# Kernel optimization log

Hardware: AMD Instinct MI355X
Metric: run time of the kernel (lower is better)

The kernel has to match this reference:

```python
import jax, jax.numpy as jnp
import numpy as np

B, T, TM = 4, 1024, 1500
D_MODEL, D_FFN, H, D_HEAD, D_MEM = 1024, 4096, 16, 64, 1024
EPS = 1e-5


def layernorm(x, g):
    m = jnp.mean(x, axis=-1, keepdims=True)
    xc = x - m
    v = jnp.mean(xc * xc, axis=-1, keepdims=True)
    return xc * jax.lax.rsqrt(v + EPS) * g


def setup_inputs() -> dict:
    key = jax.random.key(0)
    ks = jax.random.split(key, 12)
    s = lambda fan_in: 1.0 / np.sqrt(fan_in)
    return {
        "x": jax.random.normal(ks[0], (B, T, D_MODEL), jnp.float32),
        "encoder_output": jax.random.normal(ks[1], (B, TM, D_MEM), jnp.float32),
        "encoder_mask": jax.random.randint(ks[2], (B, TM), 0, 2).astype(bool),
        "w_qkv": jax.random.normal(ks[3], (D_MODEL, 3 * H * D_HEAD), jnp.float32) * s(D_MODEL),
        "w_o_sa": jax.random.normal(ks[4], (H * D_HEAD, D_MODEL), jnp.float32) * s(H * D_HEAD),
        "w_q": jax.random.normal(ks[5], (D_MODEL, H * D_HEAD), jnp.float32) * s(D_MODEL),
        "w_kv": jax.random.normal(ks[6], (D_MEM, 2 * H * D_HEAD), jnp.float32) * s(D_MEM),
        "w_o_xa": jax.random.normal(ks[7], (H * D_HEAD, D_MODEL), jnp.float32) * s(H * D_HEAD),
        "w_ff1": jax.random.normal(ks[8], (D_MODEL, D_FFN), jnp.float32) * s(D_MODEL),
        "w_ff2": jax.random.normal(ks[9], (D_FFN, D_MODEL), jnp.float32) * s(D_FFN),
        "g_sa": jnp.ones((D_MODEL,), jnp.float32),
        "g_xaq": jnp.ones((D_MODEL,), jnp.float32),
        "g_xam": jnp.ones((D_MEM,), jnp.float32),
        "g_ff": jnp.ones((D_MODEL,), jnp.float32),
    }


def reference(x, encoder_output, encoder_mask, w_qkv, w_o_sa, w_q, w_kv, w_o_xa,
              w_ff1, w_ff2, g_sa, g_xaq, g_xam, g_ff):
    b, t, _ = x.shape
    scale = D_HEAD ** -0.5

    # ---- causal self-attention ----
    residual = x
    xn = layernorm(x, g_sa)
    qkv = (xn @ w_qkv).reshape(b, t, 3, H, D_HEAD)
    q, k, v = qkv[:, :, 0], qkv[:, :, 1], qkv[:, :, 2]  # (B,T,H,D)
    scores = jnp.einsum('bqhd,bkhd->bhqk', q, k) * scale
    causal = jnp.tril(jnp.ones((t, t), x.dtype))
    scores = scores + (1.0 - causal) * -1e9
    attn = jax.nn.softmax(scores, axis=-1)
    sa = jnp.einsum('bhqk,bkhd->bqhd', attn, v).reshape(b, t, H * D_HEAD)
    x = residual + sa @ w_o_sa

    # ---- cross-attention ----
    residual = x
    qn = layernorm(x, g_xaq)
    mn = layernorm(encoder_output, g_xam)
    tq, tm = t, mn.shape[1]
    qx = (qn @ w_q).reshape(b, tq, H, D_HEAD)
    kvx = (mn @ w_kv).reshape(b, tm, 2, H, D_HEAD)
    kx, vx = kvx[:, :, 0], kvx[:, :, 1]
    xs = jnp.einsum('bqhd,bkhd->bhqk', qx, kx) * scale
    xs = jnp.where(encoder_mask[:, None, None, :], xs, -jnp.inf)
    xattn = jax.nn.softmax(xs, axis=-1)
    xa = jnp.einsum('bhqk,bkhd->bqhd', xattn, vx).reshape(b, tq, H * D_HEAD)
    x = residual + xa @ w_o_xa

    # ---- pointwise FFN (kernel_size=1 conv == linear) ----
    residual = x
    h = layernorm(x, g_ff)
    h = jax.nn.gelu(h @ w_ff1, approximate=True) @ w_ff2
    x = residual + h
    return (x, k, v)
```

## Files before the change

### kernel.cpp

```cpp
#include <hip/hip_runtime.h>
#include <hip/hip_bf16.h>
#include <cstdint>
#include <cstddef>


typedef __attribute__((ext_vector_type(4))) float f32x4;
typedef __attribute__((ext_vector_type(8))) short s8v;
typedef __attribute__((ext_vector_type(2))) unsigned uint2v;

#define DEVI __device__ __forceinline__

DEVI short f2bf(float f) {
  union { float f; unsigned u; } x; x.f = f;
  unsigned r = x.u + 0x7fffu + ((x.u >> 16) & 1u);
  return (short)(r >> 16);
}
DEVI unsigned cvtpk_bf2(float lo, float hi) {
  unsigned r;
  asm("v_cvt_pk_bf16_f32 %0, %1, %2" : "=v"(r) : "v"(lo), "v"(hi));
  return r;
}
DEVI float fexp2(float x) {
  float r;
  asm("v_exp_f32 %0, %1" : "=v"(r) : "v"(x));
  return r;
}
DEVI float fmax3(float a, float b, float c) {
  float r;
  asm("v_max3_f32 %0, %1, %2, %3" : "=v"(r) : "v"(a), "v"(b), "v"(c));
  return r;
}
DEVI float bpermf(int srclane, float v) {
  union { float f; int i; } x; x.f = v;
  x.i = __builtin_amdgcn_ds_bpermute(srclane << 2, x.i);
  return x.f;
}
DEVI void gload_lds16(const void* g, void* l) {
  __builtin_amdgcn_global_load_lds((const __attribute__((address_space(1))) void*)g,
                                   (__attribute__((address_space(3))) void*)l,
                                   16, 0, 0);
}

DEVI void xcd_swizzle(int& bx, int& by) {
  int gx = gridDim.x, gy = gridDim.y;
  int nxy = gx * gy, chunk = nxy >> 3;
  int orig = blockIdx.y * gx + blockIdx.x;
  int gid = (orig & 7) * chunk + (orig >> 3);
  int full = gy << 3, nfull = gx >> 3, lim = nfull * full;
  if (gid < lim) {
    int band = gid / full, r = gid - band * full;
    bx = (band << 3) + (r & 7);
    by = r >> 3;
  } else {
    int r = gid - lim, w = gx - (nfull << 3);
    bx = (nfull << 3) + r % w;
    by = r / w;
  }
}

__global__ __launch_bounds__(256) void k_prep(
    const float* __restrict__ wqkv, const float* __restrict__ wosa,
    const float* __restrict__ wq,   const float* __restrict__ wkv,
    const float* __restrict__ woxa, const float* __restrict__ wff1,
    const float* __restrict__ wff2,
    short* __restrict__ wqkv_t, short* __restrict__ wosa_t,
    short* __restrict__ wq_t,   short* __restrict__ wkv_t,
    short* __restrict__ woxa_t, short* __restrict__ wff1_t,
    short* __restrict__ wff2_t,
    const int* __restrict__ mask, unsigned long long* __restrict__ mbits) {
  int id = blockIdx.x;
  const float* w; short* wt; int K, N, tx, r;
  if (id < 3072)       { w = wqkv; wt = wqkv_t; K = 1024; N = 3072; tx = 96;  r = id; }
  else if (id < 4096)  { w = wosa; wt = wosa_t; K = 1024; N = 1024; tx = 32;  r = id - 3072; }
  else if (id < 5120)  { w = wq;   wt = wq_t;   K = 1024; N = 1024; tx = 32;  r = id - 4096; }
  else if (id < 7168)  { w = wkv;  wt = wkv_t;  K = 1024; N = 2048; tx = 64;  r = id - 5120; }
  else if (id < 8192)  { w = woxa; wt = woxa_t; K = 1024; N = 1024; tx = 32;  r = id - 7168; }
  else if (id < 12288) { w = wff1; wt = wff1_t; K = 1024; N = 4096; tx = 128; r = id - 8192; }
  else if (id < 16384) { w = wff2; wt = wff2_t; K = 4096; N = 1024; tx = 32;  r = id - 12288; }
  else {
    int t = threadIdx.x;
    if (t < 96) {
      int b = t / 24, wd = t % 24;
      unsigned long long v = 0;
      const int* mb = mask + (size_t)b * 1500;
      for (int j = 0; j < 64; j++) {
        int k = wd * 64 + j;
        if (k < 1500 && mb[k]) v |= (1ull << j);
      }
      mbits[b * 24 + wd] = v;
    }
    return;
  }
  __shared__ float tile[32][33];
  int n0 = (r % tx) * 32, k0 = (r / tx) * 32;
  int t = threadIdx.x;
  int row = t >> 3, c4 = (t & 7) * 4;
  *(f32x4*)&tile[row][c4] = *(const f32x4*)(w + (size_t)(k0 + row) * N + n0 + c4);
  __syncthreads();
  float v0 = tile[c4 + 0][row], v1 = tile[c4 + 1][row];
  float v2 = tile[c4 + 2][row], v3 = tile[c4 + 3][row];
  uint2v o = {cvtpk_bf2(v0, v1), cvtpk_bf2(v2, v3)};
  *(uint2v*)(wt + (size_t)(n0 + row) * K + k0 + c4) = o;
}

__global__ __launch_bounds__(256) void k_vtrans(
    const short* __restrict__ src, int srs, int coff,
    short* __restrict__ dst, int T, int Tp) {
  __shared__ short tile[32][72];
  int bh = blockIdx.y, b = bh >> 4, h = bh & 15;
  int t0 = blockIdx.x * 32;
  const short* sB = src + (size_t)b * T * srs + coff + h * 64;
  short* dB = dst + (size_t)bh * 64 * Tp;
  int t = threadIdx.x;
  int r = t >> 3, c = (t & 7) * 8;
  int tr = t0 + r; if (tr > T - 1) tr = T - 1;
  *(s8v*)&tile[r][c] = *(const s8v*)(sB + (size_t)tr * srs + c);
  __syncthreads();
  int d = t & 63, ch = t >> 6;
  s8v o;
#pragma unroll
  for (int j = 0; j < 8; j++) o[j] = tile[ch * 8 + j][d];
  *(s8v*)(dB + (size_t)d * Tp + t0 + ch * 8) = o;
}

__global__ __launch_bounds__(256) void k_ln2(
    const float* __restrict__ x, const float* __restrict__ gx,
    short* __restrict__ ox,
    const float* __restrict__ e, const float* __restrict__ ge,
    short* __restrict__ oe) {
  int id = blockIdx.x;
  const float* src; const float* g; short* dst; int row;
  if (id < 4096) { src = x; g = gx; dst = ox; row = id; }
  else           { src = e; g = ge; dst = oe; row = id - 4096; }
  const float* xr = src + (size_t)row * 1024;
  int t = threadIdx.x, wid = t >> 6, lane = t & 63;
  f32x4 v = ((const f32x4*)xr)[t];
  float s = v[0] + v[1] + v[2] + v[3];
#pragma unroll
  for (int m = 32; m >= 1; m >>= 1) s += __shfl_xor(s, m);
  __shared__ float red[4];
  if (lane == 0) red[wid] = s;
  __syncthreads();
  float mean = (red[0] + red[1] + red[2] + red[3]) * (1.f / 1024.f);
  float q = 0.f;
#pragma unroll
  for (int i = 0; i < 4; i++) { v[i] -= mean; q += v[i] * v[i]; }
#pragma unroll
  for (int m = 32; m >= 1; m >>= 1) q += __shfl_xor(q, m);
  __syncthreads();
  if (lane == 0) red[wid] = q;
  __syncthreads();
  float var = (red[0] + red[1] + red[2] + red[3]) * (1.f / 1024.f);
  float rs = rsqrtf(var + 1e-5f);
  f32x4 gv = ((const f32x4*)g)[t];
  uint2v w = {cvtpk_bf2(v[0] * rs * gv[0], v[1] * rs * gv[1]),
              cvtpk_bf2(v[2] * rs * gv[2], v[3] * rs * gv[3])};
  *(uint2v*)(dst + (size_t)row * 1024 + t * 4) = w;
}

__global__ __launch_bounds__(256) void k_ln(
    const float* __restrict__ x, const float* __restrict__ g,
    short* __restrict__ out) {
  int row = blockIdx.x;
  const float* xr = x + (size_t)row * 1024;
  int t = threadIdx.x, wid = t >> 6, lane = t & 63;
  f32x4 v = ((const f32x4*)xr)[t];
  float s = v[0] + v[1] + v[2] + v[3];
#pragma unroll
  for (int m = 32; m >= 1; m >>= 1) s += __shfl_xor(s, m);
  __shared__ float red[4];
  if (lane == 0) red[wid] = s;
  __syncthreads();
  float mean = (red[0] + red[1] + red[2] + red[3]) * (1.f / 1024.f);
  float q = 0.f;
#pragma unroll
  for (int i = 0; i < 4; i++) { v[i] -= mean; q += v[i] * v[i]; }
#pragma unroll
  for (int m = 32; m >= 1; m >>= 1) q += __shfl_xor(q, m);
  __syncthreads();
  if (lane == 0) red[wid] = q;
  __syncthreads();
  float var = (red[0] + red[1] + red[2] + red[3]) * (1.f / 1024.f);
  float rs = rsqrtf(var + 1e-5f);
  f32x4 gv = ((const f32x4*)g)[t];
  uint2v w = {cvtpk_bf2(v[0] * rs * gv[0], v[1] * rs * gv[1]),
              cvtpk_bf2(v[2] * rs * gv[2], v[3] * rs * gv[3])};
  *(uint2v*)(out + (size_t)row * 1024 + t * 4) = w;
}

template <bool GELU_, bool F32OUT, bool BF16OUT, bool KV, bool SPLIT>
__global__ __launch_bounds__(512) void k_gemm4(
    const short* __restrict__ A, const short* __restrict__ Bt,
    float* __restrict__ Cf, short* __restrict__ Cb,
    float* __restrict__ okv, int M, int N, int K, int lda, int ldb) {
  __shared__ short As[128 * 64];
  __shared__ short Bs[256 * 64];
  if (SPLIT) {
    int z = blockIdx.z;
    A += (size_t)z * K;
    Bt += (size_t)z * K;
    if (F32OUT) Cf += (size_t)z * (size_t)M * N;
  }

  int bx, by;
  xcd_swizzle(bx, by);
  int am = bx * 128, bn = by * 256;

  int t = threadIdx.x, wid = t >> 6, lane = t & 63;
  int la = lane & 15, lb = lane >> 4;
  int wr = wid >> 2, wc = wid & 3;

  const short* gpA[2]; const short* gpB[4];
  int dofA[2], dofB[4];
#pragma unroll
  for (int l = 0; l < 2; l++) {
    int c = l * 512 + t;
    int row = c >> 3, g = c & 7;
    int ar = am + row; if (ar > M - 1) ar = M - 1;
    gpA[l] = A + (size_t)ar * lda + ((g ^ (row & 7)) << 3);
    dofA[l] = (l * 512 + wid * 64) * 8;
  }
#pragma unroll
  for (int l = 0; l < 4; l++) {
    int c = l * 512 + t;
    int row = c >> 3, g = c & 7;
    gpB[l] = Bt + (size_t)(bn + row) * ldb + ((g ^ (row & 7)) << 3);
    dofB[l] = (l * 512 + wid * 64) * 8;
  }

  int aOff[4], bOff[4];
#pragma unroll
  for (int m = 0; m < 4; m++) {
    int r = wr * 64 + m * 16 + la;
    aOff[m] = r * 64 + ((lb ^ (r & 7)) << 3);
  }
#pragma unroll
  for (int n = 0; n < 4; n++) {
    int r = wc * 64 + n * 16 + la;
    bOff[n] = r * 64 + ((lb ^ (r & 7)) << 3);
  }

  f32x4 acc[4][4];
#pragma unroll
  for (int m = 0; m < 4; m++)
#pragma unroll
    for (int n = 0; n < 4; n++) acc[m][n] = (f32x4){0.f, 0.f, 0.f, 0.f};

  int nk = K >> 6;
  for (int ks = 0; ks < nk; ++ks) {
#pragma unroll
    for (int l = 0; l < 2; l++) { gload_lds16(gpA[l], As + dofA[l]); gpA[l] += 64; }
#pragma unroll
    for (int l = 0; l < 4; l++) { gload_lds16(gpB[l], Bs + dofB[l]); gpB[l] += 64; }
    __syncthreads();
#pragma unroll
    for (int kk = 0; kk < 2; kk++) {
      s8v af[4], bfg[4];
#pragma unroll
      for (int m = 0; m < 4; m++)
        af[m] = *(const s8v*)(As + (aOff[m] ^ (kk << 5)));
#pragma unroll
      for (int n = 0; n < 4; n++)
        bfg[n] = *(const s8v*)(Bs + (bOff[n] ^ (kk << 5)));
#pragma unroll
      for (int m = 0; m < 4; m++)
#pragma unroll
        for (int n = 0; n < 4; n++)
          acc[m][n] = __builtin_amdgcn_mfma_f32_16x16x32_bf16(af[m], bfg[n], acc[m][n], 0, 0, 0);
    }
    __syncthreads();
  }

#pragma unroll
  for (int m = 0; m < 4; m++) {
    int rb = am + wr * 64 + m * 16 + lb * 4;
#pragma unroll
    for (int n = 0; n < 4; n++) {
      int col = bn + wc * 64 + n * 16 + la;
#pragma unroll
      for (int j = 0; j < 4; j++) {
        int r = rb + j;
        if (r < M) {
          float v = acc[m][n][j];
          if (GELU_) {
            float u = v;
            float y = 0.7978845608f * u * (1.f + 0.044715f * u * u);
            float e = fexp2(fminf(y * 2.88539008f, 80.f));
            float th = (e - 1.f) * __builtin_amdgcn_rcpf(e + 1.f);
            v = 0.5f * u * (1.f + th);
          }
          if (F32OUT) Cf[(size_t)r * N + col] = v;
          if (BF16OUT) Cb[(size_t)r * N + col] = f2bf(v);
          if (KV) {
            if (col >= 2048)
              okv[(size_t)4096 * 1024 + (size_t)r * 1024 + (col - 2048)] = v;
            else if (col >= 1024)
              okv[(size_t)r * 1024 + (col - 1024)] = v;
          }
        }
      }
    }
  }
}

template <bool RES, bool F32OUT, bool BF16OUT>
__global__ __launch_bounds__(256) void k_gemm5(
    const short* __restrict__ A, const short* __restrict__ Bt,
    float* __restrict__ Cf, short* __restrict__ Cb,
    const float* __restrict__ res, int M, int N, int K, int lda, int ldb) {
  __shared__ short As[128 * 64];
  __shared__ short Bs[64 * 64];

  int bx, by;
  xcd_swizzle(bx, by);
  int am = bx * 128, bn = by * 64;

  int t = threadIdx.x, wid = t >> 6, lane = t & 63;
  int la = lane & 15, lb = lane >> 4;
  int wr = wid >> 1, wc = wid & 1;

  const short* gpA[4]; const short* gpB[2];
  int dofA[4], dofB[2];
#pragma unroll
  for (int l = 0; l < 4; l++) {
    int cl = l * 256 + t;
    int row = cl >> 3, g = cl & 7;
    int ar = am + row; if (ar > M - 1) ar = M - 1;
    gpA[l] = A + (size_t)ar * lda + ((g ^ (row & 7)) << 3);
    dofA[l] = (l * 256 + wid * 64) * 8;
  }
#pragma unroll
  for (int l = 0; l < 2; l++) {
    int cl = l * 256 + t;
    int row = cl >> 3, g = cl & 7;
    gpB[l] = Bt + (size_t)(bn + row) * ldb + ((g ^ (row & 7)) << 3);
    dofB[l] = (l * 256 + wid * 64) * 8;
  }

  int aOff[4], bOff[2];
#pragma unroll
  for (int m = 0; m < 4; m++) {
    int r = wr * 64 + m * 16 + la;
    aOff[m] = r * 64 + ((lb ^ (r & 7)) << 3);
  }
#pragma unroll
  for (int n = 0; n < 2; n++) {
    int r = wc * 32 + n * 16 + la;
    bOff[n] = r * 64 + ((lb ^ (r & 7)) << 3);
  }

  f32x4 acc[4][2];
#pragma unroll
  for (int m = 0; m < 4; m++)
#pragma unroll
    for (int n = 0; n < 2; n++) acc[m][n] = (f32x4){0.f, 0.f, 0.f, 0.f};

  int nk = K >> 6;
  for (int ks = 0; ks < nk; ++ks) {
#pragma unroll
    for (int l = 0; l < 4; l++) { gload_lds16(gpA[l], As + dofA[l]); gpA[l] += 64; }
#pragma unroll
    for (int l = 0; l < 2; l++) { gload_lds16(gpB[l], Bs + dofB[l]); gpB[l] += 64; }
    __syncthreads();
#pragma unroll
    for (int kk = 0; kk < 2; kk++) {
      s8v af[4], bfg[2];
#pragma unroll
      for (int m = 0; m < 4; m++)
        af[m] = *(const s8v*)(As + (aOff[m] ^ (kk << 5)));
#pragma unroll
      for (int n = 0; n < 2; n++)
        bfg[n] = *(const s8v*)(Bs + (bOff[n] ^ (kk << 5)));
#pragma unroll
      for (int m = 0; m < 4; m++)
#pragma unroll
        for (int n = 0; n < 2; n++)
          acc[m][n] = __builtin_amdgcn_mfma_f32_16x16x32_bf16(af[m], bfg[n], acc[m][n], 0, 0, 0);
    }
    __syncthreads();
  }

#pragma unroll
  for (int m = 0; m < 4; m++) {
    int rb = am + wr * 64 + m * 16 + lb * 4;
#pragma unroll
    for (int n = 0; n < 2; n++) {
      int col = bn + wc * 32 + n * 16 + la;
#pragma unroll
      for (int j = 0; j < 4; j++) {
        int r = rb + j;
        if (r < M) {
          float v = acc[m][n][j];
          if (RES) v += res[(size_t)r * N + col];
          if (F32OUT) Cf[(size_t)r * N + col] = v;
          if (BF16OUT) Cb[(size_t)r * N + col] = f2bf(v);
        }
      }
    }
  }
}

__global__ __launch_bounds__(256) void k_red4(
    const f32x4* __restrict__ p, const f32x4* __restrict__ res,
    float* __restrict__ outf, int n) {
  int i = blockIdx.x * 256 + threadIdx.x;
  f32x4 v = res[i] + ((p[i] + p[i + (size_t)n]) +
                      (p[i + 2 * (size_t)n] + p[i + 3 * (size_t)n]));
  ((f32x4*)outf)[i] = v;
}

template <bool CAUSAL>
__global__ __launch_bounds__(512) void k_attn4(
    const short* __restrict__ qbuf, int qrs,
    const short* __restrict__ kbuf, int krs,
    const short* __restrict__ vT, int vts,
    short* __restrict__ obuf, int ors,
    const unsigned long long* __restrict__ mbits, int mwords,
    int Tq, int Tk, float scale) {
  __shared__ short Ks[64 * 64];
  __shared__ short Vs[64 * 64];
  __shared__ short Ps[8 * 1024];
  int lid = blockIdx.y * gridDim.x + blockIdx.x;
  int rest = lid >> 3;
  int bh = (lid & 7) * 8 + (rest & 7);
  int qsel = rest >> 3;
  int st = CAUSAL ? (qsel < 4 ? qsel : 11 - qsel) : qsel;
  int b = bh >> 4, h = bh & 15;
  int t = threadIdx.x, wid = t >> 6, lane = t & 63;
  int la = lane & 15, lb = lane >> 4;
  float lscale = scale * 1.44269504f;

  const short* qB = qbuf + (size_t)b * Tq * qrs + h * 64;
  const short* kB = kbuf + (size_t)b * Tk * krs + h * 64;
  const short* vB = vT + (size_t)bh * 64 * vts;
  char* Pw = (char*)(Ps + wid * 1024);

  int sr = t >> 3, scol = (t & 7) * 8;
  int swz = sr * 64 + (scol ^ ((sr & 7) << 3));

  int q0 = st * 128 + wid * 16;
  int nkt = CAUSAL ? 2 * st + 2 : (Tk + 63) >> 6;
  int lastkt = CAUSAL ? (q0 >> 6) : nkt - 1;

  s8v qf[2];
#pragma unroll
  for (int kk = 0; kk < 2; kk++)
    qf[kk] = *(const s8v*)(qB + (size_t)(q0 + la) * qrs + kk * 32 + lb * 8);

  f32x4 accO[4];
#pragma unroll
  for (int n = 0; n < 4; n++) accO[n] = (f32x4){0.f, 0.f, 0.f, 0.f};
  float m = -1e30f, l = 0.f;

  s8v krg, vrg;
  {
    int tk = sr; if (tk > Tk - 1) tk = Tk - 1;
    krg = *(const s8v*)(kB + (size_t)tk * krs + scol);
    vrg = *(const s8v*)(vB + (size_t)sr * vts + scol);
  }

  for (int kt = 0; kt < nkt; kt++) {
    int kb0 = kt << 6;
    __syncthreads();
    *(s8v*)&Ks[swz] = krg;
    *(s8v*)&Vs[swz] = vrg;
    __syncthreads();
    if (kt + 1 < nkt) {
      int kb = kb0 + 64;
      int tk = kb + sr; if (tk > Tk - 1) tk = Tk - 1;
      krg = *(const s8v*)(kB + (size_t)tk * krs + scol);
      vrg = *(const s8v*)(vB + (size_t)sr * vts + kb + scol);
    }
    if (kt > lastkt) continue;

    bool needMask;
    unsigned long long wm = ~0ull;
    if (CAUSAL) {
      needMask = (kt == lastkt);
    } else {
      wm = mbits[(size_t)b * mwords + kt];
      needMask = (wm != ~0ull);
    }

    float sc[4][4];
    __builtin_amdgcn_s_setprio(1);
#pragma unroll
    for (int n = 0; n < 4; n++) {
      f32x4 a = (f32x4){0.f, 0.f, 0.f, 0.f};
#pragma unroll
      for (int kk = 0; kk < 2; kk++) {
        s8v kf = *(const s8v*)&Ks[(n * 16 + la) * 64 +
                                  ((kk * 32 + lb * 8) ^ ((la & 7) << 3))];
        a = __builtin_amdgcn_mfma_f32_16x16x32_bf16(kf, qf[kk], a, 0, 0, 0);
      }
      if (needMask) {
#pragma unroll
        for (int j = 0; j < 4; j++) {
          int ki = n * 16 + lb * 4 + j;
          bool ok = CAUSAL ? (kb0 + ki <= q0 + la) : (((wm >> ki) & 1ull) != 0);
          sc[n][j] = ok ? a[j] : -1e30f;
        }
      } else {
#pragma unroll
        for (int j = 0; j < 4; j++) sc[n][j] = a[j];
      }
    }
    __builtin_amdgcn_s_setprio(0);

    float rn[4];
#pragma unroll
    for (int n = 0; n < 4; n++)
      rn[n] = fmaxf(fmax3(sc[n][0], sc[n][1], sc[n][2]), sc[n][3]);
    float tm = fmaxf(fmax3(rn[0], rn[1], rn[2]), rn[3]);
    tm = fmaxf(tm, __shfl_xor(tm, 16));
    tm = fmaxf(tm, __shfl_xor(tm, 32));
    tm = fmaxf(tm * lscale, -1e4f);

    bool skip = __all(tm - m <= 10.f);
    float alpha = 1.f;
    if (!skip) {
      float mn_ = fmaxf(m, tm);
      alpha = fexp2(m - mn_);
      m = mn_;
    }
    float nm = -m;

    unsigned W[4][2];
    float ps = 0.f;
#pragma unroll
    for (int n = 0; n < 4; n++) {
      float p0 = fexp2(__builtin_fmaf(sc[n][0], lscale, nm));
      float p1 = fexp2(__builtin_fmaf(sc[n][1], lscale, nm));
      float p2 = fexp2(__builtin_fmaf(sc[n][2], lscale, nm));
      float p3 = fexp2(__builtin_fmaf(sc[n][3], lscale, nm));
      ps += (p0 + p1) + (p2 + p3);
      W[n][0] = cvtpk_bf2(p0, p1);
      W[n][1] = cvtpk_bf2(p2, p3);
    }
    ps += __shfl_xor(ps, 16);
    ps += __shfl_xor(ps, 32);
    l = l * alpha + ps;

    if (!skip) {
#pragma unroll
      for (int j = 0; j < 4; j++) {
        float aj = bpermf(lb * 20 + j, alpha);
#pragma unroll
        for (int n = 0; n < 4; n++) accO[n][j] *= aj;
      }
    }

#pragma unroll
    for (int n = 0; n < 4; n++) {
      uint2v w2 = {W[n][0], W[n][1]};
      *(uint2v*)(Pw + ((la * 128 + n * 32 + lb * 8) ^ ((la & 7) << 4))) = w2;
    }
    __builtin_amdgcn_s_setprio(1);
#pragma unroll
    for (int kk = 0; kk < 2; kk++) {
      s8v pa = *(const s8v*)(Pw + ((la * 128 + kk * 64 + lb * 16) ^ ((la & 7) << 4)));
#pragma unroll
      for (int n = 0; n < 4; n++) {
        s8v vf = *(const s8v*)&Vs[(n * 16 + la) * 64 +
                                  ((kk * 32 + lb * 8) ^ ((la & 7) << 3))];
        accO[n] = __builtin_amdgcn_mfma_f32_16x16x32_bf16(pa, vf, accO[n], 0, 0, 0);
      }
    }
    __builtin_amdgcn_s_setprio(0);
  }

#pragma unroll
  for (int j = 0; j < 4; j++) {
    float lj = bpermf(lb * 20 + j, l);
    float inv = 1.f / lj;
    int r = q0 + lb * 4 + j;
#pragma unroll
    for (int n = 0; n < 4; n++)
      obuf[(size_t)(b * Tq + r) * ors + h * 64 + n * 16 + la] = f2bf(accO[n][j] * inv);
  }
}

extern "C" void kernel_launch(void* const* d_in, const int* in_sizes, int n_in,
                              void* d_out, int out_size, void* d_ws, size_t ws_size,
                              hipStream_t stream) {
  (void)in_sizes; (void)n_in; (void)out_size; (void)ws_size;
  const float* x      = (const float*)d_in[0];
  const float* enc    = (const float*)d_in[1];
  const int*   mask   = (const int*)d_in[2];
  const float* w_qkv  = (const float*)d_in[3];
  const float* w_o_sa = (const float*)d_in[4];
  const float* w_q    = (const float*)d_in[5];
  const float* w_kv   = (const float*)d_in[6];
  const float* w_o_xa = (const float*)d_in[7];
  const float* w_ff1  = (const float*)d_in[8];
  const float* w_ff2  = (const float*)d_in[9];
  const float* g_sa   = (const float*)d_in[10];
  const float* g_xaq  = (const float*)d_in[11];
  const float* g_xam  = (const float*)d_in[12];
  const float* g_ff   = (const float*)d_in[13];

  float* out_x = (float*)d_out;
  float* out_k = out_x + (size_t)4096 * 1024;

  char* ws = (char*)d_ws;
  size_t off = 0;
  auto alloc = [&](size_t bytes) -> void* {
    void* p = ws + off;
    off += (bytes + 255) & ~(size_t)255;
    return p;
  };
  short* wqkv_t = (short*)alloc((size_t)3072 * 1024 * 2);
  short* wosa_t = (short*)alloc((size_t)1024 * 1024 * 2);
  short* wq_t   = (short*)alloc((size_t)1024 * 1024 * 2);
  short* wkv_t  = (short*)alloc((size_t)2048 * 1024 * 2);
  short* woxa_t = (short*)alloc((size_t)1024 * 1024 * 2);
  short* wff1_t = (short*)alloc((size_t)4096 * 1024 * 2);
  short* wff2_t = (short*)alloc((size_t)1024 * 4096 * 2);
  short* xn     = (short*)alloc((size_t)4096 * 1024 * 2);
  short* qkv_b  = (short*)alloc((size_t)4096 * 3072 * 2);
  short* sa_b   = (short*)alloc((size_t)4096 * 1024 * 2);
  float* x1     = (float*)alloc((size_t)4096 * 1024 * 4);
  short* qn     = (short*)alloc((size_t)4096 * 1024 * 2);
  short* mn     = (short*)alloc((size_t)6000 * 1024 * 2);
  short* qx_b   = (short*)alloc((size_t)4096 * 1024 * 2);
  short* kvx_b  = (short*)alloc((size_t)6000 * 2048 * 2);
  short* xa_b   = (short*)alloc((size_t)4096 * 1024 * 2);
  float* x2     = (float*)alloc((size_t)4096 * 1024 * 4);
  short* hn     = (short*)alloc((size_t)4096 * 1024 * 2);
  short* h1     = (short*)alloc((size_t)4096 * 4096 * 2);
  unsigned long long* mbits = (unsigned long long*)alloc(4 * 24 * 8);

  short* vTsa = xn;
  short* vTxa = h1;
  float* partQ = (float*)qkv_b;
  const int NRED = 1048576;

  k_prep<<<16385, 256, 0, stream>>>(
      w_qkv, w_o_sa, w_q, w_kv, w_o_xa, w_ff1, w_ff2,
      wqkv_t, wosa_t, wq_t, wkv_t, woxa_t, wff1_t, wff2_t, mask, mbits);
  k_ln2<<<10096, 256, 0, stream>>>(x, g_sa, xn, enc, g_xam, mn);

  k_gemm4<false, false, true, true, false><<<dim3(32, 12), 512, 0, stream>>>(
      xn, wqkv_t, nullptr, qkv_b, out_k, 4096, 3072, 1024, 1024, 1024);
  k_vtrans<<<dim3(32, 64), 256, 0, stream>>>(qkv_b, 3072, 2048, vTsa, 1024, 1024);
  k_attn4<true><<<dim3(8, 64), 512, 0, stream>>>(
      qkv_b, 3072, qkv_b + 1024, 3072, vTsa, 1024,
      sa_b, 1024, nullptr, 0, 1024, 1024, 0.125f);
  k_gemm5<true, true, false><<<dim3(32, 16), 256, 0, stream>>>(
      sa_b, wosa_t, x1, nullptr, x, 4096, 1024, 1024, 1024, 1024);
  k_ln<<<4096, 256, 0, stream>>>(x1, g_xaq, qn);

  k_gemm5<false, false, true><<<dim3(32, 16), 256, 0, stream>>>(
      qn, wq_t, nullptr, qx_b, nullptr, 4096, 1024, 1024, 1024, 1024);
  k_gemm4<false, false, true, false, false><<<dim3(47, 8), 512, 0, stream>>>(
      mn, wkv_t, nullptr, kvx_b, nullptr, 6000, 2048, 1024, 1024, 1024);
  k_vtrans<<<dim3(48, 64), 256, 0, stream>>>(kvx_b, 2048, 1024, vTxa, 1500, 1536);
  k_attn4<false><<<dim3(8, 64), 512, 0, stream>>>(
      qx_b, 1024, kvx_b, 2048, vTxa, 1536,
      xa_b, 1024, mbits, 24, 1024, 1500, 0.125f);
  k_gemm5<true, true, false><<<dim3(32, 16), 256, 0, stream>>>(
      xa_b, woxa_t, x2, nullptr, x1, 4096, 1024, 1024, 1024, 1024);
  k_ln<<<4096, 256, 0, stream>>>(x2, g_ff, hn);

  k_gemm4<true, false, true, false, false><<<dim3(32, 16), 512, 0, stream>>>(
      hn, wff1_t, nullptr, h1, nullptr, 4096, 4096, 1024, 1024, 1024);
  k_gemm4<false, true, false, false, true><<<dim3(32, 4, 4), 512, 0, stream>>>(
      h1, wff2_t, partQ, nullptr, nullptr, 4096, 1024, 1024, 4096, 4096);
  k_red4<<<4096, 256, 0, stream>>>(
      (const f32x4*)partQ, (const f32x4*)x2, out_x, NRED);
}
```

Before: 385.4 us.

## Split cross-attention over key range into two halves with merge kernel

Cross-attention now runs as a split-KV (flash-decoding style) pass: each block handles half of the 24 key tiles, writing unnormalised fp32 partial outputs plus running max and sum, and a new merge kernel combines the two halves with log-sum-exp weights into the bf16 output. The goal is to double the number of blocks (512 to 1024) so more of the GPU is occupied during the non-causal attention. The cost is extra fp32 partial-output traffic, a second kernel launch, and the reuse of the qkv buffer as scratch.

```diff
diff --git a/kernel.cpp b/kernel.cpp
--- a/kernel.cpp
+++ b/kernel.cpp
@@ -409,21 +409,23 @@
   ((f32x4*)outf)[i] = v;
 }
 
-template <bool CAUSAL>
+template <bool CAUSAL, bool PART>
 __global__ __launch_bounds__(512) void k_attn4(
     const short* __restrict__ qbuf, int qrs,
     const short* __restrict__ kbuf, int krs,
     const short* __restrict__ vT, int vts,
     short* __restrict__ obuf, int ors,
+    float* __restrict__ Opf, float* __restrict__ mlf,
     const unsigned long long* __restrict__ mbits, int mwords,
     int Tq, int Tk, float scale) {
   __shared__ short Ks[64 * 64];
   __shared__ short Vs[64 * 64];
   __shared__ short Ps[8 * 1024];
   int lid = blockIdx.y * gridDim.x + blockIdx.x;
-  int rest = lid >> 3;
-  int bh = (lid & 7) * 8 + (rest & 7);
-  int qsel = rest >> 3;
+  int bh = (lid & 7) * 8 + ((lid >> 3) & 7);
+  int r2 = lid >> 6;
+  int qsel = PART ? (r2 & 7) : r2;
+  int half = PART ? (r2 >> 3) : 0;
   int st = CAUSAL ? (qsel < 4 ? qsel : 11 - qsel) : qsel;
   int b = bh >> 4, h = bh & 15;
   int t = threadIdx.x, wid = t >> 6, lane = t & 63;
@@ -439,8 +441,9 @@
   int swz = sr * 64 + (scol ^ ((sr & 7) << 3));
 
   int q0 = st * 128 + wid * 16;
-  int nkt = CAUSAL ? 2 * st + 2 : (Tk + 63) >> 6;
-  int lastkt = CAUSAL ? (q0 >> 6) : nkt - 1;
+  int ktbase = PART ? half * 12 : 0;
+  int nkt = CAUSAL ? 2 * st + 2 : (PART ? 12 : (Tk + 63) >> 6);
+  int lastkt = CAUSAL ? (q0 >> 6) : (ktbase + nkt - 1);
 
   s8v qf[2];
 #pragma unroll
@@ -454,13 +457,14 @@
 
   s8v krg, vrg;
   {
-    int tk = sr; if (tk > Tk - 1) tk = Tk - 1;
+    int tk = ktbase * 64 + sr; if (tk > Tk - 1) tk = Tk - 1;
     krg = *(const s8v*)(kB + (size_t)tk * krs + scol);
-    vrg = *(const s8v*)(vB + (size_t)sr * vts + scol);
+    vrg = *(const s8v*)(vB + (size_t)sr * vts + ktbase * 64 + scol);
   }
 
   for (int kt = 0; kt < nkt; kt++) {
-    int kb0 = kt << 6;
+    int g = ktbase + kt;
+    int kb0 = g << 6;
     __syncthreads();
     *(s8v*)&Ks[swz] = krg;
     *(s8v*)&Vs[swz] = vrg;
@@ -471,14 +475,14 @@
       krg = *(const s8v*)(kB + (size_t)tk * krs + scol);
       vrg = *(const s8v*)(vB + (size_t)sr * vts + kb + scol);
     }
-    if (kt > lastkt) continue;
+    if (g > lastkt) continue;
 
     bool needMask;
     unsigned long long wm = ~0ull;
     if (CAUSAL) {
-      needMask = (kt == lastkt);
+      needMask = (g == lastkt);
     } else {
-      wm = mbits[(size_t)b * mwords + kt];
+      wm = mbits[(size_t)b * mwords + g];
       needMask = (wm != ~0ull);
     }
 
@@ -569,15 +573,47 @@
     __builtin_amdgcn_s_setprio(0);
   }
 
-#pragma unroll
-  for (int j = 0; j < 4; j++) {
-    float lj = bpermf(lb * 20 + j, l);
-    float inv = 1.f / lj;
-    int r = q0 + lb * 4 + j;
-#pragma unroll
-    for (int n = 0; n < 4; n++)
-      obuf[(size_t)(b * Tq + r) * ors + h * 64 + n * 16 + la] = f2bf(accO[n][j] * inv);
-  }
+  if (PART) {
+    size_t rowb = ((size_t)half * 64 + bh) * 1024;
+#pragma unroll
+    for (int j = 0; j < 4; j++) {
+      int r = q0 + lb * 4 + j;
+#pragma unroll
+      for (int n = 0; n < 4; n++)
+        Opf[(rowb + r) * 64 + n * 16 + la] = accO[n][j];
+    }
+    if (lb == 0) {
+      mlf[(rowb + q0 + la) * 2]     = m;
+      mlf[(rowb + q0 + la) * 2 + 1] = l;
+    }
+  } else {
+#pragma unroll
+    for (int j = 0; j < 4; j++) {
+      float lj = bpermf(lb * 20 + j, l);
+      float inv = 1.f / lj;
+      int r = q0 + lb * 4 + j;
+#pragma unroll
+      for (int n = 0; n < 4; n++)
+        obuf[(size_t)(b * Tq + r) * ors + h * 64 + n * 16 + la] = f2bf(accO[n][j] * inv);
+    }
+  }
+}
+
+__global__ __launch_bounds__(256) void k_amerge(
+    const float* __restrict__ Opf, const float* __restrict__ mlf,
+    short* __restrict__ out) {
+  size_t i = (size_t)blockIdx.x * 256 + threadIdx.x;
+  int d = (int)(i & 63);
+  size_t row = i >> 6;
+  float m0 = mlf[row * 2], l0 = mlf[row * 2 + 1];
+  float m1 = mlf[(row + 65536) * 2], l1 = mlf[(row + 65536) * 2 + 1];
+  float mm = fmaxf(m0, m1);
+  float w0 = fexp2(m0 - mm), w1 = fexp2(m1 - mm);
+  float inv = 1.f / (l0 * w0 + l1 * w1);
+  float o = (Opf[i] * w0 + Opf[i + (size_t)4194304] * w1) * inv;
+  int bh = (int)(row >> 10), qr = (int)(row & 1023);
+  int b = bh >> 4, h = bh & 15;
+  out[((size_t)(b * 1024 + qr)) * 1024 + h * 64 + d] = f2bf(o);
 }
 
 extern "C" void kernel_launch(void* const* d_in, const int* in_sizes, int n_in,
@@ -629,10 +665,12 @@
   short* hn     = (short*)alloc((size_t)4096 * 1024 * 2);
   short* h1     = (short*)alloc((size_t)4096 * 4096 * 2);
   unsigned long long* mbits = (unsigned long long*)alloc(4 * 24 * 8);
+  float* mlbuf  = (float*)alloc((size_t)2 * 65536 * 2 * 4);
 
   short* vTsa = xn;
   short* vTxa = h1;
   float* partQ = (float*)qkv_b;
+  float* partA = (float*)qkv_b;
   const int NRED = 1048576;
 
   k_prep<<<16385, 256, 0, stream>>>(
@@ -643,9 +681,9 @@
   k_gemm4<false, false, true, true, false><<<dim3(32, 12), 512, 0, stream>>>(
       xn, wqkv_t, nullptr, qkv_b, out_k, 4096, 3072, 1024, 1024, 1024);
   k_vtrans<<<dim3(32, 64), 256, 0, stream>>>(qkv_b, 3072, 2048, vTsa, 1024, 1024);
-  k_attn4<true><<<dim3(8, 64), 512, 0, stream>>>(
+  k_attn4<true, false><<<dim3(8, 64), 512, 0, stream>>>(
       qkv_b, 3072, qkv_b + 1024, 3072, vTsa, 1024,
-      sa_b, 1024, nullptr, 0, 1024, 1024, 0.125f);
+      sa_b, 1024, nullptr, nullptr, nullptr, 0, 1024, 1024, 0.125f);
   k_gemm5<true, true, false><<<dim3(32, 16), 256, 0, stream>>>(
       sa_b, wosa_t, x1, nullptr, x, 4096, 1024, 1024, 1024, 1024);
   k_ln<<<4096, 256, 0, stream>>>(x1, g_xaq, qn);
@@ -655,9 +693,10 @@
   k_gemm4<false, false, true, false, false><<<dim3(47, 8), 512, 0, stream>>>(
       mn, wkv_t, nullptr, kvx_b, nullptr, 6000, 2048, 1024, 1024, 1024);
   k_vtrans<<<dim3(48, 64), 256, 0, stream>>>(kvx_b, 2048, 1024, vTxa, 1500, 1536);
-  k_attn4<false><<<dim3(8, 64), 512, 0, stream>>>(
+  k_attn4<false, true><<<dim3(16, 64), 512, 0, stream>>>(
       qx_b, 1024, kvx_b, 2048, vTxa, 1536,
-      xa_b, 1024, mbits, 24, 1024, 1500, 0.125f);
+      nullptr, 0, partA, mlbuf, mbits, 24, 1024, 1500, 0.125f);
+  k_amerge<<<16384, 256, 0, stream>>>(partA, mlbuf, xa_b);
   k_gemm5<true, true, false><<<dim3(32, 16), 256, 0, stream>>>(
       xa_b, woxa_t, x2, nullptr, x1, 4096, 1024, 1024, 1024, 1024);
   k_ln<<<4096, 256, 0, stream>>>(x2, g_ff, hn);
```

Result: slower. 395.8 us (+2.7%).
